# Kernel tuning notes

Hardware: AMD Instinct MI355X
Metric: run time of the kernel (lower is better)

## Reference

```python
import jax, jax.numpy as jnp
import numpy as np

N = 500_000   # mesh vertices
M = 500_000   # non-manifold sample points
K = 4         # quad-mesh valence
WEIGHTS = [7000.0, 600.0, 10.0, 50.0, 30.0, 3.0]


def setup_inputs() -> dict:
    key = jax.random.key(0)
    ks = jax.random.split(key, 11)
    return {
        "manifold_pred": jax.random.normal(ks[0], (1, N), jnp.float32),
        "nonmanifold_pred": jax.random.normal(ks[1], (1, M), jnp.float32),
        "mnfld_grad": jax.random.normal(ks[2], (1, N, 3), jnp.float32),
        "nonmnfld_grad": jax.random.normal(ks[3], (1, M, 3), jnp.float32),
        "mnfld_hessian": jax.random.normal(ks[4], (1, N, 3, 3), jnp.float32),
        "mnfld_n_gt": jax.random.normal(ks[5], (1, N, 3), jnp.float32),
        "theta": jax.random.normal(ks[6], (1, N, 1), jnp.float32),
        "local_coord_u": jax.random.normal(ks[7], (1, N, 3), jnp.float32),
        "local_coord_v": jax.random.normal(ks[8], (1, N, 3), jnp.float32),
        "rot": jax.random.normal(ks[9], (N, K, 3, 3), jnp.float32),
        "neighbors": jax.random.randint(ks[10], (N, K), 0, N, jnp.int32),
    }


def reference(manifold_pred, nonmanifold_pred, mnfld_grad, nonmnfld_grad,
              mnfld_hessian, mnfld_n_gt, theta, local_coord_u, local_coord_v,
              rot, neighbors):
    H = mnfld_hessian[0]          # [N,3,3] per-vertex hessian
    n_gt = mnfld_n_gt[0]          # [N,3]

    # morse term: n^T H  (div_type == 'l1')
    morse = 0.5 * jnp.abs(jnp.einsum('nd,nde->ne', n_gt, H)).mean()

    sdf_term = jnp.abs(manifold_pred).mean()

    # eikonal over concatenated grads (morse path uses nonmnfld_grad when near_points is None)
    all_grads = jnp.concatenate([nonmnfld_grad, mnfld_grad], axis=-2)  # [1, M+N, 3]
    eikonal_term = jnp.abs(jnp.linalg.norm(all_grads, axis=2) - 1.0).mean()

    inter_term = jnp.exp(-100.0 * jnp.abs(nonmanifold_pred)).mean()

    # cross-field directions from theta
    u, v, th = local_coord_u[0], local_coord_v[0], theta[0]  # [N,3],[N,3],[N,1]
    va = u * jnp.cos(th) + v * jnp.sin(th)
    va = va / (jnp.linalg.norm(va, axis=-1, keepdims=True) + 1e-12)
    vb = -u * jnp.sin(th) + v * jnp.cos(th)
    vb = vb / (jnp.linalg.norm(vb, axis=-1, keepdims=True) + 1e-12)

    # per-vertex (v^T H) x v hessian alignment (single valence group covers all vertices)
    vaH = jnp.einsum('nd,nde->ne', va, H)
    vbH = jnp.einsum('nd,nde->ne', vb, H)
    h_alpha = jnp.abs(jnp.cross(vaH, va)).mean()
    h_beta = jnp.abs(jnp.cross(vbH, vb)).mean()
    theta_hessian_term = 0.5 * (h_alpha + h_beta)

    # neighbor consistency: rotate neighbor cross-field into vertex frame, dot products
    vaj = jnp.einsum('nkij,nkj->nki', rot, va[neighbors])  # [N,K,3]
    vbj = jnp.einsum('nkij,nkj->nki', rot, vb[neighbors])
    aa = jnp.abs(jnp.einsum('nd,nkd->nk', va, vaj))
    ab = jnp.abs(jnp.einsum('nd,nkd->nk', va, vbj))
    ba = jnp.abs(jnp.einsum('nd,nkd->nk', vb, vaj))
    bb = jnp.abs(jnp.einsum('nd,nkd->nk', vb, vbj))
    theta_neighbors_term = (aa + ab + ba + bb - 2.0).mean()

    w = WEIGHTS
    loss = (w[0] * sdf_term + w[1] * inter_term + w[3] * eikonal_term
            + w[5] * morse + w[2] * theta_hessian_term + w[4] * theta_neighbors_term)
    return jnp.stack([loss, sdf_term, inter_term, eikonal_term, morse,
                      theta_hessian_term, theta_neighbors_term])
```

## Files before the change

### kernel.cpp

```cpp
#include <hip/hip_runtime.h>
#include <math.h>

static constexpr int BLOCK = 256;
static constexpr int WAVES = BLOCK / 64;
static constexpr int KVAL = 4;
static constexpr int TILE = 256;

typedef float f4 __attribute__((ext_vector_type(4)));
typedef int i4 __attribute__((ext_vector_type(4)));
typedef int i2 __attribute__((ext_vector_type(2)));
typedef unsigned int u2v __attribute__((ext_vector_type(2)));

__device__ __forceinline__ void norm3(float x, float y, float z,
                                      float& ox, float& oy, float& oz) {
  float inv = 1.0f / (sqrtf(x * x + y * y + z * z) + 1e-12f);
  ox = x * inv; oy = y * inv; oz = z * inv;
}

template <int NV>
__device__ __forceinline__ void block_reduce(float (&p)[NV]) {
#pragma unroll
  for (int off = 32; off > 0; off >>= 1)
#pragma unroll
    for (int q = 0; q < NV; ++q) p[q] += __shfl_down(p[q], off, 64);
  __shared__ float sm[WAVES][NV];
  int wave = threadIdx.x >> 6, lane = threadIdx.x & 63;
  if (lane == 0)
#pragma unroll
    for (int q = 0; q < NV; ++q) sm[wave][q] = p[q];
  __syncthreads();
  if (threadIdx.x == 0) {
#pragma unroll
    for (int q = 0; q < NV; ++q) {
      float t = 0.f;
#pragma unroll
      for (int w = 1; w < WAVES; ++w) t += sm[w][q];
      p[q] += t;
    }
  }
}

__device__ __forceinline__ void stage_f(float* __restrict__ dst,
                                        const float* __restrict__ src, int nf) {
  int t = threadIdx.x;
  int nf4 = nf >> 2;
  const f4* s4 = (const f4*)src;
  f4* d4 = (f4*)dst;
  for (int i = t; i < nf4; i += BLOCK) d4[i] = s4[i];
  int rem = nf & 3;
  if (t < rem) dst[nf4 * 4 + t] = src[nf4 * 4 + t];
}

__device__ __forceinline__ void stage_rot_pad(float* __restrict__ B,
                                              const float* __restrict__ src,
                                              int cs) {
  int nf4 = 9 * cs;
  const f4* s4 = (const f4*)src;
  for (int i = threadIdx.x; i < nf4; i += BLOCK) {
    f4 x = __builtin_nontemporal_load(s4 + i);
    int vtx = i / 9, r = i - 9 * vtx;
    float* d = B + vtx * 37 + r * 4;
    d[0] = x.x; d[1] = x.y; d[2] = x.z; d[3] = x.w;
  }
}

__device__ __forceinline__ void unpack8(u2v w, float* va, float* vb) {
  va[0] = __builtin_amdgcn_cvt_f32_fp8((int)w.x, 0);
  va[1] = __builtin_amdgcn_cvt_f32_fp8((int)w.x, 1);
  va[2] = __builtin_amdgcn_cvt_f32_fp8((int)w.x, 2);
  vb[0] = __builtin_amdgcn_cvt_f32_fp8((int)w.x, 3);
  vb[1] = __builtin_amdgcn_cvt_f32_fp8((int)w.y, 0);
  vb[2] = __builtin_amdgcn_cvt_f32_fp8((int)w.y, 1);
}

__global__ __launch_bounds__(BLOCK) void s1_kernel(
    const float* __restrict__ theta, const float* __restrict__ u,
    const float* __restrict__ v, u2v* __restrict__ vavb8, int N,
    const float* __restrict__ pred, const float* __restrict__ pgrad,
    const float* __restrict__ mp, const float* __restrict__ grad,
    const float* __restrict__ H, const float* __restrict__ ngt,
    float* __restrict__ part1, int nb1, int M) {
  __shared__ float B[2304];
  int t = threadIdx.x;
  long base = (long)blockIdx.x * TILE;
  float p[5] = {0.f, 0.f, 0.f, 0.f, 0.f};

  int cntM = 0, cntN = 0;
  if (base < M) { long c = (long)M - base; cntM = c > TILE ? TILE : (int)c; }
  if (base < N) { long c = (long)N - base; cntN = c > TILE ? TILE : (int)c; }

  float prv = 0.f, mpv = 0.f, thv = 0.f;
  if (t < cntM) prv = pred[base + t];
  if (t < cntN) { mpv = mp[base + t]; thv = theta[base + t]; }

  if (cntM > 0) stage_f(B, pgrad + 3 * base, 3 * cntM);
  __syncthreads();
  if (t < cntM) {
    float gx = B[3 * t], gy = B[3 * t + 1], gz = B[3 * t + 2];
    p[1] += fabsf(sqrtf(gx * gx + gy * gy + gz * gz) - 1.0f);
    p[4] += __expf(-100.0f * fabsf(prv));
  }
  __syncthreads();
  float ng0 = 0.f, ng1 = 0.f, ng2 = 0.f;
  if (cntN > 0) {
    stage_f(B, grad + 3 * base, 3 * cntN);
    stage_f(B + 768, ngt + 3 * base, 3 * cntN);
  }
  __syncthreads();
  if (t < cntN) {
    float gx = B[3 * t], gy = B[3 * t + 1], gz = B[3 * t + 2];
    p[1] += fabsf(sqrtf(gx * gx + gy * gy + gz * gz) - 1.0f);
    p[0] = fabsf(mpv);
    ng0 = B[768 + 3 * t]; ng1 = B[768 + 3 * t + 1]; ng2 = B[768 + 3 * t + 2];
  }
  __syncthreads();

  if (cntN > 0) {
    stage_f(B, u + 3 * base, 3 * cntN);
    stage_f(B + 768, v + 3 * base, 3 * cntN);
  }
  __syncthreads();
  float va[3] = {0.f, 0.f, 0.f}, vb[3] = {0.f, 0.f, 0.f};
  if (t < cntN) {
    float s, c;
    __sincosf(thv, &s, &c);
    float ux = B[3 * t], uy = B[3 * t + 1], uz = B[3 * t + 2];
    float vx = B[768 + 3 * t], vy = B[768 + 3 * t + 1], vz = B[768 + 3 * t + 2];
    norm3(ux * c + vx * s, uy * c + vy * s, uz * c + vz * s, va[0], va[1], va[2]);
    norm3(vx * c - ux * s, vy * c - uy * s, vz * c - uz * s, vb[0], vb[1], vb[2]);
    unsigned int w0 = (unsigned)__builtin_amdgcn_cvt_pk_fp8_f32(va[0], va[1], 0, false);
    w0 = (unsigned)__builtin_amdgcn_cvt_pk_fp8_f32(va[2], vb[0], (int)w0, true);
    unsigned int w1 = (unsigned)__builtin_amdgcn_cvt_pk_fp8_f32(vb[1], vb[2], 0, false);
    u2v o; o.x = w0; o.y = w1;
    __builtin_nontemporal_store(o, &vavb8[base + t]);
  }
  __syncthreads();

  if (cntN > 0) stage_f(B, H + 9 * base, 9 * cntN);
  __syncthreads();
  if (t < cntN) {
    float h[9];
#pragma unroll
    for (int q = 0; q < 9; ++q) h[q] = B[9 * t + q];
    p[2] = fabsf(ng0 * h[0] + ng1 * h[3] + ng2 * h[6]) +
           fabsf(ng0 * h[1] + ng1 * h[4] + ng2 * h[7]) +
           fabsf(ng0 * h[2] + ng1 * h[5] + ng2 * h[8]);
    float a0 = va[0] * h[0] + va[1] * h[3] + va[2] * h[6];
    float a1 = va[0] * h[1] + va[1] * h[4] + va[2] * h[7];
    float a2 = va[0] * h[2] + va[1] * h[5] + va[2] * h[8];
    float b0 = vb[0] * h[0] + vb[1] * h[3] + vb[2] * h[6];
    float b1 = vb[0] * h[1] + vb[1] * h[4] + vb[2] * h[7];
    float b2 = vb[0] * h[2] + vb[1] * h[5] + vb[2] * h[8];
    p[3] = fabsf(a1 * va[2] - a2 * va[1]) + fabsf(a2 * va[0] - a0 * va[2]) +
           fabsf(a0 * va[1] - a1 * va[0]) + fabsf(b1 * vb[2] - b2 * vb[1]) +
           fabsf(b2 * vb[0] - b0 * vb[2]) + fabsf(b0 * vb[1] - b1 * vb[0]);
  }

  block_reduce<5>(p);
  if (t == 0) {
#pragma unroll
    for (int q = 0; q < 5; ++q) part1[q * nb1 + blockIdx.x] = p[q];
  }
}

__global__ __launch_bounds__(BLOCK) void s3_kernel(
    const u2v* __restrict__ vavb8, const float* __restrict__ rot,
    const i2* __restrict__ nbr2, float* __restrict__ part2, int N) {
  __shared__ float B[128 * 37];
  int t = threadIdx.x;
  int vl = t >> 1;
  int h = t & 1;
  long base = (long)blockIdx.x * TILE;
  int cntN = 0;
  if (base < N) { long c = (long)N - base; cntN = c > TILE ? TILE : (int)c; }

  u2v wn[2][2]; u2v ws[2];
#pragma unroll
  for (int sp = 0; sp < 2; ++sp) {
    ws[sp] = u2v{0, 0};
    wn[sp][0] = u2v{0, 0};
    wn[sp][1] = u2v{0, 0};
    int lv = 128 * sp + vl;
    if (lv < cntN) {
      long n = base + lv;
      i2 jj = __builtin_nontemporal_load(&nbr2[2 * n + h]);
      wn[sp][0] = vavb8[jj.x];
      wn[sp][1] = vavb8[jj.y];
      ws[sp] = vavb8[n];
    }
  }

  float nsum = 0.f;
#pragma unroll
  for (int sp = 0; sp < 2; ++sp) {
    int cs = cntN - 128 * sp;
    if (cs < 0) cs = 0;
    if (cs > 128) cs = 128;
    if (cs > 0) stage_rot_pad(B, rot + 36 * (base + 128 * sp), cs);
    __syncthreads();
    if (vl < cs) {
      float va[3], vb[3];
      unpack8(ws[sp], va, vb);
      const float* R0 = B + 37 * vl;
#pragma unroll
      for (int kk = 0; kk < 2; ++kk) {
        int k = 2 * h + kk;
        float R[9];
#pragma unroll
        for (int q = 0; q < 9; ++q) R[q] = R0[9 * k + q];
        float pa0 = R[0] * va[0] + R[3] * va[1] + R[6] * va[2];
        float pa1 = R[1] * va[0] + R[4] * va[1] + R[7] * va[2];
        float pa2 = R[2] * va[0] + R[5] * va[1] + R[8] * va[2];
        float pb0 = R[0] * vb[0] + R[3] * vb[1] + R[6] * vb[2];
        float pb1 = R[1] * vb[0] + R[4] * vb[1] + R[7] * vb[2];
        float pb2 = R[2] * vb[0] + R[5] * vb[1] + R[8] * vb[2];
        float aj[3], bj[3];
        unpack8(wn[sp][kk], aj, bj);
        nsum += fabsf(pa0 * aj[0] + pa1 * aj[1] + pa2 * aj[2]) +
                fabsf(pa0 * bj[0] + pa1 * bj[1] + pa2 * bj[2]) +
                fabsf(pb0 * aj[0] + pb1 * aj[1] + pb2 * aj[2]) +
                fabsf(pb0 * bj[0] + pb1 * bj[1] + pb2 * bj[2]) - 2.0f;
      }
    }
    __syncthreads();
  }
  float p[1] = {nsum};
  block_reduce<1>(p);
  if (t == 0) part2[blockIdx.x] = p[0];
}

__global__ __launch_bounds__(BLOCK) void finalize_fast(
    const float* __restrict__ part1, int nb1, const float* __restrict__ part2,
    int nb2, float* __restrict__ out, int N, int M) {
  float s[6] = {0.f, 0.f, 0.f, 0.f, 0.f, 0.f};
  for (int b = threadIdx.x; b < nb1; b += BLOCK) {
#pragma unroll
    for (int q = 0; q < 5; ++q) s[q] += part1[q * nb1 + b];
  }
  for (int b = threadIdx.x; b < nb2; b += BLOCK) s[5] += part2[b];
  block_reduce<6>(s);
  if (threadIdx.x == 0) {
    float sdf = s[0] / (float)N;
    float eik = s[1] / (float)(N + M);
    float morse = 0.5f * s[2] / (3.0f * (float)N);
    float th = 0.5f * s[3] / (3.0f * (float)N);
    float inter = s[4] / (float)M;
    float nb = s[5] / ((float)N * (float)KVAL);
    float loss = 7000.0f * sdf + 600.0f * inter + 50.0f * eik + 3.0f * morse +
                 10.0f * th + 30.0f * nb;
    out[0] = loss; out[1] = sdf; out[2] = inter; out[3] = eik;
    out[4] = morse; out[5] = th; out[6] = nb;
  }
}

__device__ __forceinline__ void crossfield(const float* __restrict__ u,
                                           const float* __restrict__ v,
                                           const float* __restrict__ theta,
                                           int n, float va[3], float vb[3]) {
  float s, c;
  __sincosf(theta[n], &s, &c);
  float ux = u[3 * n], uy = u[3 * n + 1], uz = u[3 * n + 2];
  float vx = v[3 * n], vy = v[3 * n + 1], vz = v[3 * n + 2];
  norm3(ux * c + vx * s, uy * c + vy * s, uz * c + vz * s, va[0], va[1], va[2]);
  norm3(vx * c - ux * s, vy * c - uy * s, vz * c - uz * s, vb[0], vb[1], vb[2]);
}

__global__ __launch_bounds__(BLOCK) void vertex_kernel(
    const float* __restrict__ mp, const float* __restrict__ grad,
    const float* __restrict__ H, const float* __restrict__ ngt,
    const float* __restrict__ theta, const float* __restrict__ u,
    const float* __restrict__ v, const float* __restrict__ rot,
    const int* __restrict__ nbr, float* __restrict__ acc, int N) {
  int n = blockIdx.x * blockDim.x + threadIdx.x;
  float p[5] = {0.f, 0.f, 0.f, 0.f, 0.f};
  if (n < N) {
    float hh[9];
#pragma unroll
    for (int i = 0; i < 9; ++i) hh[i] = H[9 * (size_t)n + i];
    p[0] = fabsf(mp[n]);
    float gx = grad[3 * n], gy = grad[3 * n + 1], gz = grad[3 * n + 2];
    p[1] = fabsf(sqrtf(gx * gx + gy * gy + gz * gz) - 1.0f);
    float n0 = ngt[3 * n], n1 = ngt[3 * n + 1], n2 = ngt[3 * n + 2];
    p[2] = fabsf(n0 * hh[0] + n1 * hh[3] + n2 * hh[6]) +
           fabsf(n0 * hh[1] + n1 * hh[4] + n2 * hh[7]) +
           fabsf(n0 * hh[2] + n1 * hh[5] + n2 * hh[8]);
    float va[3], vb[3];
    crossfield(u, v, theta, n, va, vb);
    {
      float a0 = va[0] * hh[0] + va[1] * hh[3] + va[2] * hh[6];
      float a1 = va[0] * hh[1] + va[1] * hh[4] + va[2] * hh[7];
      float a2 = va[0] * hh[2] + va[1] * hh[5] + va[2] * hh[8];
      float b0 = vb[0] * hh[0] + vb[1] * hh[3] + vb[2] * hh[6];
      float b1 = vb[0] * hh[1] + vb[1] * hh[4] + vb[2] * hh[7];
      float b2 = vb[0] * hh[2] + vb[1] * hh[5] + vb[2] * hh[8];
      p[3] = fabsf(a1 * va[2] - a2 * va[1]) + fabsf(a2 * va[0] - a0 * va[2]) +
             fabsf(a0 * va[1] - a1 * va[0]) + fabsf(b1 * vb[2] - b2 * vb[1]) +
             fabsf(b2 * vb[0] - b0 * vb[2]) + fabsf(b0 * vb[1] - b1 * vb[0]);
    }
    float nsum = 0.f;
    const float* R = rot + (size_t)n * (KVAL * 9);
#pragma unroll
    for (int k = 0; k < KVAL; ++k) {
      int j = nbr[KVAL * (size_t)n + k];
      float vaj[3], vbj[3];
      crossfield(u, v, theta, j, vaj, vbj);
      float r0 = R[9 * k + 0], r1 = R[9 * k + 1], r2 = R[9 * k + 2];
      float r3 = R[9 * k + 3], r4 = R[9 * k + 4], r5 = R[9 * k + 5];
      float r6 = R[9 * k + 6], r7 = R[9 * k + 7], r8 = R[9 * k + 8];
      float wa0 = r0 * vaj[0] + r1 * vaj[1] + r2 * vaj[2];
      float wa1 = r3 * vaj[0] + r4 * vaj[1] + r5 * vaj[2];
      float wa2 = r6 * vaj[0] + r7 * vaj[1] + r8 * vaj[2];
      float wb0 = r0 * vbj[0] + r1 * vbj[1] + r2 * vbj[2];
      float wb1 = r3 * vbj[0] + r4 * vbj[1] + r5 * vbj[2];
      float wb2 = r6 * vbj[0] + r7 * vbj[1] + r8 * vbj[2];
      nsum += fabsf(va[0] * wa0 + va[1] * wa1 + va[2] * wa2) +
              fabsf(va[0] * wb0 + va[1] * wb1 + va[2] * wb2) +
              fabsf(vb[0] * wa0 + vb[1] * wa1 + vb[2] * wa2) +
              fabsf(vb[0] * wb0 + vb[1] * wb1 + vb[2] * wb2) - 2.0f;
    }
    p[4] = nsum;
  }
  block_reduce<5>(p);
  if (threadIdx.x == 0) {
    atomicAdd(&acc[0], p[0]); atomicAdd(&acc[1], p[1]); atomicAdd(&acc[2], p[2]);
    atomicAdd(&acc[3], p[3]); atomicAdd(&acc[4], p[4]);
  }
}

__global__ __launch_bounds__(BLOCK) void point_kernel(
    const float* __restrict__ pred, const float* __restrict__ grad,
    float* __restrict__ acc, int M) {
  int i = blockIdx.x * blockDim.x + threadIdx.x;
  float p[2] = {0.f, 0.f};
  if (i < M) {
    p[0] = __expf(-100.0f * fabsf(pred[i]));
    float gx = grad[3 * i], gy = grad[3 * i + 1], gz = grad[3 * i + 2];
    p[1] = fabsf(sqrtf(gx * gx + gy * gy + gz * gz) - 1.0f);
  }
  block_reduce<2>(p);
  if (threadIdx.x == 0) {
    atomicAdd(&acc[5], p[0]); atomicAdd(&acc[1], p[1]);
  }
}

__global__ void finalize_acc(const float* __restrict__ acc, float* __restrict__ out,
                             int N, int M) {
  if (threadIdx.x == 0 && blockIdx.x == 0) {
    float sdf = acc[0] / (float)N;
    float eik = acc[1] / (float)(N + M);
    float morse = 0.5f * acc[2] / (3.0f * (float)N);
    float th = 0.5f * acc[3] / (3.0f * (float)N);
    float nb = acc[4] / ((float)N * (float)KVAL);
    float inter = acc[5] / (float)M;
    float loss = 7000.0f * sdf + 600.0f * inter + 50.0f * eik + 3.0f * morse +
                 10.0f * th + 30.0f * nb;
    out[0] = loss; out[1] = sdf; out[2] = inter; out[3] = eik;
    out[4] = morse; out[5] = th; out[6] = nb;
  }
}

extern "C" void kernel_launch(void* const* d_in, const int* in_sizes, int n_in,
                              void* d_out, int out_size, void* d_ws, size_t ws_size,
                              hipStream_t stream) {
  const float* mp    = (const float*)d_in[0];
  const float* npred = (const float*)d_in[1];
  const float* grad  = (const float*)d_in[2];
  const float* ngrad = (const float*)d_in[3];
  const float* H     = (const float*)d_in[4];
  const float* ngt   = (const float*)d_in[5];
  const float* theta = (const float*)d_in[6];
  const float* u     = (const float*)d_in[7];
  const float* v     = (const float*)d_in[8];
  const float* rot   = (const float*)d_in[9];
  const int*   nbr   = (const int*)d_in[10];
  float* out = (float*)d_out;

  int N = in_sizes[0];
  int M = in_sizes[1];
  int mx = (N > M) ? N : M;
  int nb1 = (mx + TILE - 1) / TILE;
  int nb2 = (N + TILE - 1) / TILE;

  size_t off_vavb = 256;
  size_t off_p1 = off_vavb + (size_t)N * 8;
  size_t off_p2 = off_p1 + (size_t)5 * nb1 * 4;
  size_t need = off_p2 + (size_t)nb2 * 4;

  if (ws_size >= need) {
    u2v* vavb8   = (u2v*)((char*)d_ws + off_vavb);
    float* part1 = (float*)((char*)d_ws + off_p1);
    float* part2 = (float*)((char*)d_ws + off_p2);
    s1_kernel<<<nb1, BLOCK, 0, stream>>>(
        theta, u, v, vavb8, N, npred, ngrad, mp, grad, H, ngt, part1, nb1, M);
    s3_kernel<<<nb2, BLOCK, 0, stream>>>(
        vavb8, rot, (const i2*)nbr, part2, N);
    finalize_fast<<<1, BLOCK, 0, stream>>>(part1, nb1, part2, nb2, out, N, M);
  } else {
    float* acc = (float*)d_ws;
    (void)hipMemsetAsync(acc, 0, 6 * sizeof(float), stream);
    vertex_kernel<<<(N + BLOCK - 1) / BLOCK, BLOCK, 0, stream>>>(
        mp, grad, H, ngt, theta, u, v, rot, nbr, acc, N);
    point_kernel<<<(M + BLOCK - 1) / BLOCK, BLOCK, 0, stream>>>(npred, ngrad, acc, M);
    finalize_acc<<<1, 64, 0, stream>>>(acc, out, N, M);
  }
}
```

Before: 51.24 us.

## Split crossfield into small prepass and fuse stream terms with neighbor term

Moves crossfield computation (theta, u, v to fp8 va/vb) into a small first kernel. The streaming loss terms (sdf, eikonal, inter, morse, hessian) and the neighbor-consistency term now run together in one main kernel. That kernel issues the neighbor gathers early, so their latency overlaps with the streaming of H and the gradients. It also uses one thread per vertex with an int4 neighbor load, replacing two threads per vertex. The per-vertex va/vb for the hessian term now come from the fp8-packed values, which lowers that term's precision. The main kernel uses more shared memory (about 19KB), which may reduce occupancy.

```diff
diff --git a/kernel.cpp b/kernel.cpp
--- a/kernel.cpp
+++ b/kernel.cpp
@@ -8,7 +8,6 @@
 
 typedef float f4 __attribute__((ext_vector_type(4)));
 typedef int i4 __attribute__((ext_vector_type(4)));
-typedef int i2 __attribute__((ext_vector_type(2)));
 typedef unsigned int u2v __attribute__((ext_vector_type(2)));
 
 __device__ __forceinline__ void norm3(float x, float y, float z,
@@ -73,59 +72,27 @@
   vb[2] = __builtin_amdgcn_cvt_f32_fp8((int)w.y, 1);
 }
 
-__global__ __launch_bounds__(BLOCK) void s1_kernel(
+__global__ __launch_bounds__(BLOCK) void cf_kernel(
     const float* __restrict__ theta, const float* __restrict__ u,
-    const float* __restrict__ v, u2v* __restrict__ vavb8, int N,
-    const float* __restrict__ pred, const float* __restrict__ pgrad,
-    const float* __restrict__ mp, const float* __restrict__ grad,
-    const float* __restrict__ H, const float* __restrict__ ngt,
-    float* __restrict__ part1, int nb1, int M) {
-  __shared__ float B[2304];
+    const float* __restrict__ v, u2v* __restrict__ vavb8, int N) {
+  __shared__ float B[1536];
   int t = threadIdx.x;
   long base = (long)blockIdx.x * TILE;
-  float p[5] = {0.f, 0.f, 0.f, 0.f, 0.f};
-
-  int cntM = 0, cntN = 0;
-  if (base < M) { long c = (long)M - base; cntM = c > TILE ? TILE : (int)c; }
-  if (base < N) { long c = (long)N - base; cntN = c > TILE ? TILE : (int)c; }
-
-  float prv = 0.f, mpv = 0.f, thv = 0.f;
-  if (t < cntM) prv = pred[base + t];
-  if (t < cntN) { mpv = mp[base + t]; thv = theta[base + t]; }
-
-  if (cntM > 0) stage_f(B, pgrad + 3 * base, 3 * cntM);
-  __syncthreads();
-  if (t < cntM) {
-    float gx = B[3 * t], gy = B[3 * t + 1], gz = B[3 * t + 2];
-    p[1] += fabsf(sqrtf(gx * gx + gy * gy + gz * gz) - 1.0f);
-    p[4] += __expf(-100.0f * fabsf(prv));
-  }
-  __syncthreads();
-  float ng0 = 0.f, ng1 = 0.f, ng2 = 0.f;
-  if (cntN > 0) {
-    stage_f(B, grad + 3 * base, 3 * cntN);
-    stage_f(B + 768, ngt + 3 * base, 3 * cntN);
-  }
-  __syncthreads();
-  if (t < cntN) {
-    float gx = B[3 * t], gy = B[3 * t + 1], gz = B[3 * t + 2];
-    p[1] += fabsf(sqrtf(gx * gx + gy * gy + gz * gz) - 1.0f);
-    p[0] = fabsf(mpv);
-    ng0 = B[768 + 3 * t]; ng1 = B[768 + 3 * t + 1]; ng2 = B[768 + 3 * t + 2];
-  }
-  __syncthreads();
-
-  if (cntN > 0) {
-    stage_f(B, u + 3 * base, 3 * cntN);
-    stage_f(B + 768, v + 3 * base, 3 * cntN);
-  }
-  __syncthreads();
-  float va[3] = {0.f, 0.f, 0.f}, vb[3] = {0.f, 0.f, 0.f};
-  if (t < cntN) {
+  int cnt = 0;
+  if (base < N) { long c = (long)N - base; cnt = c > TILE ? TILE : (int)c; }
+  float thv = 0.f;
+  if (t < cnt) thv = theta[base + t];
+  if (cnt > 0) {
+    stage_f(B, u + 3 * base, 3 * cnt);
+    stage_f(B + 768, v + 3 * base, 3 * cnt);
+  }
+  __syncthreads();
+  if (t < cnt) {
     float s, c;
     __sincosf(thv, &s, &c);
     float ux = B[3 * t], uy = B[3 * t + 1], uz = B[3 * t + 2];
     float vx = B[768 + 3 * t], vy = B[768 + 3 * t + 1], vz = B[768 + 3 * t + 2];
+    float va[3], vb[3];
     norm3(ux * c + vx * s, uy * c + vy * s, uz * c + vz * s, va[0], va[1], va[2]);
     norm3(vx * c - ux * s, vy * c - uy * s, vz * c - uz * s, vb[0], vb[1], vb[2]);
     unsigned int w0 = (unsigned)__builtin_amdgcn_cvt_pk_fp8_f32(va[0], va[1], 0, false);
@@ -133,6 +100,63 @@
     unsigned int w1 = (unsigned)__builtin_amdgcn_cvt_pk_fp8_f32(vb[1], vb[2], 0, false);
     u2v o; o.x = w0; o.y = w1;
     __builtin_nontemporal_store(o, &vavb8[base + t]);
+  }
+}
+
+__global__ __launch_bounds__(BLOCK) void main_kernel(
+    const u2v* __restrict__ vavb8, int N,
+    const float* __restrict__ pred, const float* __restrict__ pgrad,
+    const float* __restrict__ mp, const float* __restrict__ grad,
+    const float* __restrict__ H, const float* __restrict__ ngt,
+    const float* __restrict__ rot, const i4* __restrict__ nbr4,
+    float* __restrict__ part, int nbb, int M) {
+  __shared__ float B[4736];
+  int t = threadIdx.x;
+  long base = (long)blockIdx.x * TILE;
+  float p[6] = {0.f, 0.f, 0.f, 0.f, 0.f, 0.f};
+
+  int cntM = 0, cntN = 0;
+  if (base < M) { long c = (long)M - base; cntM = c > TILE ? TILE : (int)c; }
+  if (base < N) { long c = (long)N - base; cntN = c > TILE ? TILE : (int)c; }
+
+  float prv = 0.f, mpv = 0.f;
+  u2v ws = u2v{0, 0};
+  u2v wn[4];
+#pragma unroll
+  for (int k = 0; k < KVAL; ++k) wn[k] = u2v{0, 0};
+  if (t < cntM) prv = pred[base + t];
+  if (t < cntN) {
+    mpv = mp[base + t];
+    ws = vavb8[base + t];
+    i4 jj = __builtin_nontemporal_load(&nbr4[base + t]);
+    wn[0] = vavb8[jj.x];
+    wn[1] = vavb8[jj.y];
+    wn[2] = vavb8[jj.z];
+    wn[3] = vavb8[jj.w];
+  }
+  float va[3], vb[3];
+  unpack8(ws, va, vb);
+
+  if (cntM > 0) stage_f(B, pgrad + 3 * base, 3 * cntM);
+  __syncthreads();
+  if (t < cntM) {
+    float gx = B[3 * t], gy = B[3 * t + 1], gz = B[3 * t + 2];
+    p[1] += fabsf(sqrtf(gx * gx + gy * gy + gz * gz) - 1.0f);
+    p[4] += __expf(-100.0f * fabsf(prv));
+  }
+  __syncthreads();
+
+  float ng0 = 0.f, ng1 = 0.f, ng2 = 0.f;
+  if (cntN > 0) {
+    stage_f(B, grad + 3 * base, 3 * cntN);
+    stage_f(B + 768, ngt + 3 * base, 3 * cntN);
+  }
+  __syncthreads();
+  if (t < cntN) {
+    float gx = B[3 * t], gy = B[3 * t + 1], gz = B[3 * t + 2];
+    p[1] += fabsf(sqrtf(gx * gx + gy * gy + gz * gz) - 1.0f);
+    p[0] = fabsf(mpv);
+    ng0 = B[768 + 3 * t]; ng1 = B[768 + 3 * t + 1]; ng2 = B[768 + 3 * t + 2];
   }
   __syncthreads();
 
@@ -155,40 +179,7 @@
            fabsf(a0 * va[1] - a1 * va[0]) + fabsf(b1 * vb[2] - b2 * vb[1]) +
            fabsf(b2 * vb[0] - b0 * vb[2]) + fabsf(b0 * vb[1] - b1 * vb[0]);
   }
-
-  block_reduce<5>(p);
-  if (t == 0) {
-#pragma unroll
-    for (int q = 0; q < 5; ++q) part1[q * nb1 + blockIdx.x] = p[q];
-  }
-}
-
-__global__ __launch_bounds__(BLOCK) void s3_kernel(
-    const u2v* __restrict__ vavb8, const float* __restrict__ rot,
-    const i2* __restrict__ nbr2, float* __restrict__ part2, int N) {
-  __shared__ float B[128 * 37];
-  int t = threadIdx.x;
-  int vl = t >> 1;
-  int h = t & 1;
-  long base = (long)blockIdx.x * TILE;
-  int cntN = 0;
-  if (base < N) { long c = (long)N - base; cntN = c > TILE ? TILE : (int)c; }
-
-  u2v wn[2][2]; u2v ws[2];
-#pragma unroll
-  for (int sp = 0; sp < 2; ++sp) {
-    ws[sp] = u2v{0, 0};
-    wn[sp][0] = u2v{0, 0};
-    wn[sp][1] = u2v{0, 0};
-    int lv = 128 * sp + vl;
-    if (lv < cntN) {
-      long n = base + lv;
-      i2 jj = __builtin_nontemporal_load(&nbr2[2 * n + h]);
-      wn[sp][0] = vavb8[jj.x];
-      wn[sp][1] = vavb8[jj.y];
-      ws[sp] = vavb8[n];
-    }
-  }
+  __syncthreads();
 
   float nsum = 0.f;
 #pragma unroll
@@ -198,13 +189,11 @@
     if (cs > 128) cs = 128;
     if (cs > 0) stage_rot_pad(B, rot + 36 * (base + 128 * sp), cs);
     __syncthreads();
-    if (vl < cs) {
-      float va[3], vb[3];
-      unpack8(ws[sp], va, vb);
-      const float* R0 = B + 37 * vl;
-#pragma unroll
-      for (int kk = 0; kk < 2; ++kk) {
-        int k = 2 * h + kk;
+    int lt = t - 128 * sp;
+    if (lt >= 0 && lt < cs) {
+      const float* R0 = B + 37 * lt;
+#pragma unroll
+      for (int k = 0; k < KVAL; ++k) {
         float R[9];
 #pragma unroll
         for (int q = 0; q < 9; ++q) R[q] = R0[9 * k + q];
@@ -215,7 +204,7 @@
         float pb1 = R[1] * vb[0] + R[4] * vb[1] + R[7] * vb[2];
         float pb2 = R[2] * vb[0] + R[5] * vb[1] + R[8] * vb[2];
         float aj[3], bj[3];
-        unpack8(wn[sp][kk], aj, bj);
+        unpack8(wn[k], aj, bj);
         nsum += fabsf(pa0 * aj[0] + pa1 * aj[1] + pa2 * aj[2]) +
                 fabsf(pa0 * bj[0] + pa1 * bj[1] + pa2 * bj[2]) +
                 fabsf(pb0 * aj[0] + pb1 * aj[1] + pb2 * aj[2]) +
@@ -224,20 +213,23 @@
     }
     __syncthreads();
   }
-  float p[1] = {nsum};
-  block_reduce<1>(p);
-  if (t == 0) part2[blockIdx.x] = p[0];
+  p[5] = nsum;
+
+  block_reduce<6>(p);
+  if (t == 0) {
+#pragma unroll
+    for (int q = 0; q < 6; ++q) part[q * nbb + blockIdx.x] = p[q];
+  }
 }
 
 __global__ __launch_bounds__(BLOCK) void finalize_fast(
-    const float* __restrict__ part1, int nb1, const float* __restrict__ part2,
-    int nb2, float* __restrict__ out, int N, int M) {
+    const float* __restrict__ part, int nbb, float* __restrict__ out,
+    int N, int M) {
   float s[6] = {0.f, 0.f, 0.f, 0.f, 0.f, 0.f};
-  for (int b = threadIdx.x; b < nb1; b += BLOCK) {
-#pragma unroll
-    for (int q = 0; q < 5; ++q) s[q] += part1[q * nb1 + b];
-  }
-  for (int b = threadIdx.x; b < nb2; b += BLOCK) s[5] += part2[b];
+  for (int b = threadIdx.x; b < nbb; b += BLOCK) {
+#pragma unroll
+    for (int q = 0; q < 6; ++q) s[q] += part[q * nbb + b];
+  }
   block_reduce<6>(s);
   if (threadIdx.x == 0) {
     float sdf = s[0] / (float)N;
@@ -378,23 +370,21 @@
   int N = in_sizes[0];
   int M = in_sizes[1];
   int mx = (N > M) ? N : M;
-  int nb1 = (mx + TILE - 1) / TILE;
-  int nb2 = (N + TILE - 1) / TILE;
+  int nbN = (N + TILE - 1) / TILE;
+  int nbb = (mx + TILE - 1) / TILE;
 
   size_t off_vavb = 256;
-  size_t off_p1 = off_vavb + (size_t)N * 8;
-  size_t off_p2 = off_p1 + (size_t)5 * nb1 * 4;
-  size_t need = off_p2 + (size_t)nb2 * 4;
+  size_t off_p = off_vavb + (size_t)N * 8;
+  size_t need = off_p + (size_t)6 * nbb * 4;
 
   if (ws_size >= need) {
-    u2v* vavb8   = (u2v*)((char*)d_ws + off_vavb);
-    float* part1 = (float*)((char*)d_ws + off_p1);
-    float* part2 = (float*)((char*)d_ws + off_p2);
-    s1_kernel<<<nb1, BLOCK, 0, stream>>>(
-        theta, u, v, vavb8, N, npred, ngrad, mp, grad, H, ngt, part1, nb1, M);
-    s3_kernel<<<nb2, BLOCK, 0, stream>>>(
-        vavb8, rot, (const i2*)nbr, part2, N);
-    finalize_fast<<<1, BLOCK, 0, stream>>>(part1, nb1, part2, nb2, out, N, M);
+    u2v* vavb8  = (u2v*)((char*)d_ws + off_vavb);
+    float* part = (float*)((char*)d_ws + off_p);
+    cf_kernel<<<nbN, BLOCK, 0, stream>>>(theta, u, v, vavb8, N);
+    main_kernel<<<nbb, BLOCK, 0, stream>>>(
+        vavb8, N, npred, ngrad, mp, grad, H, ngt, rot, (const i4*)nbr,
+        part, nbb, M);
+    finalize_fast<<<1, BLOCK, 0, stream>>>(part, nbb, out, N, M);
   } else {
     float* acc = (float*)d_ws;
     (void)hipMemsetAsync(acc, 0, 6 * sizeof(float), stream);
```

After: 53.79 us. 5.0% more time.

## Split crossfield into small kernel and merge reductions with neighbor pass

Applied to the files above, without the earlier changes.

Moves the crossfield computation (theta, u, v to packed fp8 va/vb) into a small first kernel. The per-point reductions and the neighbor-consistency pass now run together in one interleaved kernel: even blocks do the reductions and odd blocks do the neighbor term. The goal is to cut the serial dependency so the heavy streaming reductions overlap with the rot/gather neighbor work instead of waiting behind them. In exchange the reduction path reloads va/vb from the fp8 buffer, which adds extra reads and extra fp8 quantization in the hessian term. It also raises shared memory per block to the larger of the two paths.

```diff
diff --git a/kernel.cpp b/kernel.cpp
--- a/kernel.cpp
+++ b/kernel.cpp
@@ -73,59 +73,27 @@
   vb[2] = __builtin_amdgcn_cvt_f32_fp8((int)w.y, 1);
 }
 
-__global__ __launch_bounds__(BLOCK) void s1_kernel(
+__global__ __launch_bounds__(BLOCK) void cf_kernel(
     const float* __restrict__ theta, const float* __restrict__ u,
-    const float* __restrict__ v, u2v* __restrict__ vavb8, int N,
-    const float* __restrict__ pred, const float* __restrict__ pgrad,
-    const float* __restrict__ mp, const float* __restrict__ grad,
-    const float* __restrict__ H, const float* __restrict__ ngt,
-    float* __restrict__ part1, int nb1, int M) {
-  __shared__ float B[2304];
+    const float* __restrict__ v, u2v* __restrict__ vavb8, int N) {
+  __shared__ float B[1536];
   int t = threadIdx.x;
   long base = (long)blockIdx.x * TILE;
-  float p[5] = {0.f, 0.f, 0.f, 0.f, 0.f};
-
-  int cntM = 0, cntN = 0;
-  if (base < M) { long c = (long)M - base; cntM = c > TILE ? TILE : (int)c; }
-  if (base < N) { long c = (long)N - base; cntN = c > TILE ? TILE : (int)c; }
-
-  float prv = 0.f, mpv = 0.f, thv = 0.f;
-  if (t < cntM) prv = pred[base + t];
-  if (t < cntN) { mpv = mp[base + t]; thv = theta[base + t]; }
-
-  if (cntM > 0) stage_f(B, pgrad + 3 * base, 3 * cntM);
+  int cnt = 0;
+  if (base < N) { long c = (long)N - base; cnt = c > TILE ? TILE : (int)c; }
+  float thv = 0.f;
+  if (t < cnt) thv = theta[base + t];
+  if (cnt > 0) {
+    stage_f(B, u + 3 * base, 3 * cnt);
+    stage_f(B + 768, v + 3 * base, 3 * cnt);
+  }
   __syncthreads();
-  if (t < cntM) {
-    float gx = B[3 * t], gy = B[3 * t + 1], gz = B[3 * t + 2];
-    p[1] += fabsf(sqrtf(gx * gx + gy * gy + gz * gz) - 1.0f);
-    p[4] += __expf(-100.0f * fabsf(prv));
-  }
-  __syncthreads();
-  float ng0 = 0.f, ng1 = 0.f, ng2 = 0.f;
-  if (cntN > 0) {
-    stage_f(B, grad + 3 * base, 3 * cntN);
-    stage_f(B + 768, ngt + 3 * base, 3 * cntN);
-  }
-  __syncthreads();
-  if (t < cntN) {
-    float gx = B[3 * t], gy = B[3 * t + 1], gz = B[3 * t + 2];
-    p[1] += fabsf(sqrtf(gx * gx + gy * gy + gz * gz) - 1.0f);
-    p[0] = fabsf(mpv);
-    ng0 = B[768 + 3 * t]; ng1 = B[768 + 3 * t + 1]; ng2 = B[768 + 3 * t + 2];
-  }
-  __syncthreads();
-
-  if (cntN > 0) {
-    stage_f(B, u + 3 * base, 3 * cntN);
-    stage_f(B + 768, v + 3 * base, 3 * cntN);
-  }
-  __syncthreads();
-  float va[3] = {0.f, 0.f, 0.f}, vb[3] = {0.f, 0.f, 0.f};
-  if (t < cntN) {
+  if (t < cnt) {
     float s, c;
     __sincosf(thv, &s, &c);
     float ux = B[3 * t], uy = B[3 * t + 1], uz = B[3 * t + 2];
     float vx = B[768 + 3 * t], vy = B[768 + 3 * t + 1], vz = B[768 + 3 * t + 2];
+    float va[3], vb[3];
     norm3(ux * c + vx * s, uy * c + vy * s, uz * c + vz * s, va[0], va[1], va[2]);
     norm3(vx * c - ux * s, vy * c - uy * s, vz * c - uz * s, vb[0], vb[1], vb[2]);
     unsigned int w0 = (unsigned)__builtin_amdgcn_cvt_pk_fp8_f32(va[0], va[1], 0, false);
@@ -134,110 +102,149 @@
     u2v o; o.x = w0; o.y = w1;
     __builtin_nontemporal_store(o, &vavb8[base + t]);
   }
-  __syncthreads();
-
-  if (cntN > 0) stage_f(B, H + 9 * base, 9 * cntN);
-  __syncthreads();
-  if (t < cntN) {
-    float h[9];
-#pragma unroll
-    for (int q = 0; q < 9; ++q) h[q] = B[9 * t + q];
-    p[2] = fabsf(ng0 * h[0] + ng1 * h[3] + ng2 * h[6]) +
-           fabsf(ng0 * h[1] + ng1 * h[4] + ng2 * h[7]) +
-           fabsf(ng0 * h[2] + ng1 * h[5] + ng2 * h[8]);
-    float a0 = va[0] * h[0] + va[1] * h[3] + va[2] * h[6];
-    float a1 = va[0] * h[1] + va[1] * h[4] + va[2] * h[7];
-    float a2 = va[0] * h[2] + va[1] * h[5] + va[2] * h[8];
-    float b0 = vb[0] * h[0] + vb[1] * h[3] + vb[2] * h[6];
-    float b1 = vb[0] * h[1] + vb[1] * h[4] + vb[2] * h[7];
-    float b2 = vb[0] * h[2] + vb[1] * h[5] + vb[2] * h[8];
-    p[3] = fabsf(a1 * va[2] - a2 * va[1]) + fabsf(a2 * va[0] - a0 * va[2]) +
-           fabsf(a0 * va[1] - a1 * va[0]) + fabsf(b1 * vb[2] - b2 * vb[1]) +
-           fabsf(b2 * vb[0] - b0 * vb[2]) + fabsf(b0 * vb[1] - b1 * vb[0]);
-  }
-
-  block_reduce<5>(p);
-  if (t == 0) {
-#pragma unroll
-    for (int q = 0; q < 5; ++q) part1[q * nb1 + blockIdx.x] = p[q];
-  }
-}
-
-__global__ __launch_bounds__(BLOCK) void s3_kernel(
-    const u2v* __restrict__ vavb8, const float* __restrict__ rot,
-    const i2* __restrict__ nbr2, float* __restrict__ part2, int N) {
-  __shared__ float B[128 * 37];
+}
+
+__global__ __launch_bounds__(BLOCK) void mega_kernel(
+    const u2v* __restrict__ vavb8, int N,
+    const float* __restrict__ pred, const float* __restrict__ pgrad,
+    const float* __restrict__ mp, const float* __restrict__ grad,
+    const float* __restrict__ H, const float* __restrict__ ngt,
+    const float* __restrict__ rot, const i2* __restrict__ nbr2,
+    float* __restrict__ part1, float* __restrict__ part2, int nT, int M) {
+  __shared__ float B[4736];
   int t = threadIdx.x;
-  int vl = t >> 1;
-  int h = t & 1;
-  long base = (long)blockIdx.x * TILE;
-  int cntN = 0;
-  if (base < N) { long c = (long)N - base; cntN = c > TILE ? TILE : (int)c; }
-
-  u2v wn[2][2]; u2v ws[2];
-#pragma unroll
-  for (int sp = 0; sp < 2; ++sp) {
-    ws[sp] = u2v{0, 0};
-    wn[sp][0] = u2v{0, 0};
-    wn[sp][1] = u2v{0, 0};
-    int lv = 128 * sp + vl;
-    if (lv < cntN) {
-      long n = base + lv;
-      i2 jj = __builtin_nontemporal_load(&nbr2[2 * n + h]);
-      wn[sp][0] = vavb8[jj.x];
-      wn[sp][1] = vavb8[jj.y];
-      ws[sp] = vavb8[n];
-    }
-  }
-
-  float nsum = 0.f;
-#pragma unroll
-  for (int sp = 0; sp < 2; ++sp) {
-    int cs = cntN - 128 * sp;
-    if (cs < 0) cs = 0;
-    if (cs > 128) cs = 128;
-    if (cs > 0) stage_rot_pad(B, rot + 36 * (base + 128 * sp), cs);
+  int tile = blockIdx.x >> 1;
+  long base = (long)tile * TILE;
+
+  if ((blockIdx.x & 1) == 0) {
+    float p[5] = {0.f, 0.f, 0.f, 0.f, 0.f};
+    int cntM = 0, cntN = 0;
+    if (base < M) { long c = (long)M - base; cntM = c > TILE ? TILE : (int)c; }
+    if (base < N) { long c = (long)N - base; cntN = c > TILE ? TILE : (int)c; }
+
+    float prv = 0.f, mpv = 0.f;
+    u2v ws = u2v{0, 0};
+    if (t < cntM) prv = pred[base + t];
+    if (t < cntN) { mpv = mp[base + t]; ws = vavb8[base + t]; }
+    float va[3], vb[3];
+    unpack8(ws, va, vb);
+
+    if (cntM > 0) stage_f(B, pgrad + 3 * base, 3 * cntM);
     __syncthreads();
-    if (vl < cs) {
-      float va[3], vb[3];
-      unpack8(ws[sp], va, vb);
-      const float* R0 = B + 37 * vl;
-#pragma unroll
-      for (int kk = 0; kk < 2; ++kk) {
-        int k = 2 * h + kk;
-        float R[9];
-#pragma unroll
-        for (int q = 0; q < 9; ++q) R[q] = R0[9 * k + q];
-        float pa0 = R[0] * va[0] + R[3] * va[1] + R[6] * va[2];
-        float pa1 = R[1] * va[0] + R[4] * va[1] + R[7] * va[2];
-        float pa2 = R[2] * va[0] + R[5] * va[1] + R[8] * va[2];
-        float pb0 = R[0] * vb[0] + R[3] * vb[1] + R[6] * vb[2];
-        float pb1 = R[1] * vb[0] + R[4] * vb[1] + R[7] * vb[2];
-        float pb2 = R[2] * vb[0] + R[5] * vb[1] + R[8] * vb[2];
-        float aj[3], bj[3];
-        unpack8(wn[sp][kk], aj, bj);
-        nsum += fabsf(pa0 * aj[0] + pa1 * aj[1] + pa2 * aj[2]) +
-                fabsf(pa0 * bj[0] + pa1 * bj[1] + pa2 * bj[2]) +
-                fabsf(pb0 * aj[0] + pb1 * aj[1] + pb2 * aj[2]) +
-                fabsf(pb0 * bj[0] + pb1 * bj[1] + pb2 * bj[2]) - 2.0f;
+    if (t < cntM) {
+      float gx = B[3 * t], gy = B[3 * t + 1], gz = B[3 * t + 2];
+      p[1] += fabsf(sqrtf(gx * gx + gy * gy + gz * gz) - 1.0f);
+      p[4] += __expf(-100.0f * fabsf(prv));
+    }
+    __syncthreads();
+    float ng0 = 0.f, ng1 = 0.f, ng2 = 0.f;
+    if (cntN > 0) {
+      stage_f(B, grad + 3 * base, 3 * cntN);
+      stage_f(B + 768, ngt + 3 * base, 3 * cntN);
+    }
+    __syncthreads();
+    if (t < cntN) {
+      float gx = B[3 * t], gy = B[3 * t + 1], gz = B[3 * t + 2];
+      p[1] += fabsf(sqrtf(gx * gx + gy * gy + gz * gz) - 1.0f);
+      p[0] = fabsf(mpv);
+      ng0 = B[768 + 3 * t]; ng1 = B[768 + 3 * t + 1]; ng2 = B[768 + 3 * t + 2];
+    }
+    __syncthreads();
+    if (cntN > 0) stage_f(B, H + 9 * base, 9 * cntN);
+    __syncthreads();
+    if (t < cntN) {
+      float h[9];
+#pragma unroll
+      for (int q = 0; q < 9; ++q) h[q] = B[9 * t + q];
+      p[2] = fabsf(ng0 * h[0] + ng1 * h[3] + ng2 * h[6]) +
+             fabsf(ng0 * h[1] + ng1 * h[4] + ng2 * h[7]) +
+             fabsf(ng0 * h[2] + ng1 * h[5] + ng2 * h[8]);
+      float a0 = va[0] * h[0] + va[1] * h[3] + va[2] * h[6];
+      float a1 = va[0] * h[1] + va[1] * h[4] + va[2] * h[7];
+      float a2 = va[0] * h[2] + va[1] * h[5] + va[2] * h[8];
+      float b0 = vb[0] * h[0] + vb[1] * h[3] + vb[2] * h[6];
+      float b1 = vb[0] * h[1] + vb[1] * h[4] + vb[2] * h[7];
+      float b2 = vb[0] * h[2] + vb[1] * h[5] + vb[2] * h[8];
+      p[3] = fabsf(a1 * va[2] - a2 * va[1]) + fabsf(a2 * va[0] - a0 * va[2]) +
+             fabsf(a0 * va[1] - a1 * va[0]) + fabsf(b1 * vb[2] - b2 * vb[1]) +
+             fabsf(b2 * vb[0] - b0 * vb[2]) + fabsf(b0 * vb[1] - b1 * vb[0]);
+    }
+    block_reduce<5>(p);
+    if (t == 0) {
+#pragma unroll
+      for (int q = 0; q < 5; ++q) part1[q * nT + tile] = p[q];
+    }
+  } else {
+    int vl = t >> 1;
+    int h = t & 1;
+    int cntN = 0;
+    if (base < N) { long c = (long)N - base; cntN = c > TILE ? TILE : (int)c; }
+
+    u2v wn[2][2]; u2v ws[2];
+#pragma unroll
+    for (int sp = 0; sp < 2; ++sp) {
+      ws[sp] = u2v{0, 0};
+      wn[sp][0] = u2v{0, 0};
+      wn[sp][1] = u2v{0, 0};
+      int lv = 128 * sp + vl;
+      if (lv < cntN) {
+        long n = base + lv;
+        i2 jj = __builtin_nontemporal_load(&nbr2[2 * n + h]);
+        wn[sp][0] = vavb8[jj.x];
+        wn[sp][1] = vavb8[jj.y];
+        ws[sp] = vavb8[n];
       }
     }
-    __syncthreads();
-  }
-  float p[1] = {nsum};
-  block_reduce<1>(p);
-  if (t == 0) part2[blockIdx.x] = p[0];
+
+    float nsum = 0.f;
+#pragma unroll
+    for (int sp = 0; sp < 2; ++sp) {
+      int cs = cntN - 128 * sp;
+      if (cs < 0) cs = 0;
+      if (cs > 128) cs = 128;
+      if (cs > 0) stage_rot_pad(B, rot + 36 * (base + 128 * sp), cs);
+      __syncthreads();
+      if (vl < cs) {
+        float va[3], vb[3];
+        unpack8(ws[sp], va, vb);
+        const float* R0 = B + 37 * vl;
+#pragma unroll
+        for (int kk = 0; kk < 2; ++kk) {
+          int k = 2 * h + kk;
+          float R[9];
+#pragma unroll
+          for (int q = 0; q < 9; ++q) R[q] = R0[9 * k + q];
+          float pa0 = R[0] * va[0] + R[3] * va[1] + R[6] * va[2];
+          float pa1 = R[1] * va[0] + R[4] * va[1] + R[7] * va[2];
+          float pa2 = R[2] * va[0] + R[5] * va[1] + R[8] * va[2];
+          float pb0 = R[0] * vb[0] + R[3] * vb[1] + R[6] * vb[2];
+          float pb1 = R[1] * vb[0] + R[4] * vb[1] + R[7] * vb[2];
+          float pb2 = R[2] * vb[0] + R[5] * vb[1] + R[8] * vb[2];
+          float aj[3], bj[3];
+          unpack8(wn[sp][kk], aj, bj);
+          nsum += fabsf(pa0 * aj[0] + pa1 * aj[1] + pa2 * aj[2]) +
+                  fabsf(pa0 * bj[0] + pa1 * bj[1] + pa2 * bj[2]) +
+                  fabsf(pb0 * aj[0] + pb1 * aj[1] + pb2 * aj[2]) +
+                  fabsf(pb0 * bj[0] + pb1 * bj[1] + pb2 * bj[2]) - 2.0f;
+        }
+      }
+      __syncthreads();
+    }
+    float p[1] = {nsum};
+    block_reduce<1>(p);
+    if (t == 0) part2[tile] = p[0];
+  }
 }
 
 __global__ __launch_bounds__(BLOCK) void finalize_fast(
-    const float* __restrict__ part1, int nb1, const float* __restrict__ part2,
-    int nb2, float* __restrict__ out, int N, int M) {
+    const float* __restrict__ part1, const float* __restrict__ part2, int nT,
+    float* __restrict__ out, int N, int M) {
   float s[6] = {0.f, 0.f, 0.f, 0.f, 0.f, 0.f};
-  for (int b = threadIdx.x; b < nb1; b += BLOCK) {
-#pragma unroll
-    for (int q = 0; q < 5; ++q) s[q] += part1[q * nb1 + b];
-  }
-  for (int b = threadIdx.x; b < nb2; b += BLOCK) s[5] += part2[b];
+  for (int b = threadIdx.x; b < nT; b += BLOCK) {
+#pragma unroll
+    for (int q = 0; q < 5; ++q) s[q] += part1[q * nT + b];
+    s[5] += part2[b];
+  }
   block_reduce<6>(s);
   if (threadIdx.x == 0) {
     float sdf = s[0] / (float)N;
@@ -378,23 +385,23 @@
   int N = in_sizes[0];
   int M = in_sizes[1];
   int mx = (N > M) ? N : M;
-  int nb1 = (mx + TILE - 1) / TILE;
-  int nb2 = (N + TILE - 1) / TILE;
+  int nT = (mx + TILE - 1) / TILE;
+  int nbN = (N + TILE - 1) / TILE;
 
   size_t off_vavb = 256;
   size_t off_p1 = off_vavb + (size_t)N * 8;
-  size_t off_p2 = off_p1 + (size_t)5 * nb1 * 4;
-  size_t need = off_p2 + (size_t)nb2 * 4;
+  size_t off_p2 = off_p1 + (size_t)5 * nT * 4;
+  size_t need = off_p2 + (size_t)nT * 4;
 
   if (ws_size >= need) {
     u2v* vavb8   = (u2v*)((char*)d_ws + off_vavb);
     float* part1 = (float*)((char*)d_ws + off_p1);
     float* part2 = (float*)((char*)d_ws + off_p2);
-    s1_kernel<<<nb1, BLOCK, 0, stream>>>(
-        theta, u, v, vavb8, N, npred, ngrad, mp, grad, H, ngt, part1, nb1, M);
-    s3_kernel<<<nb2, BLOCK, 0, stream>>>(
-        vavb8, rot, (const i2*)nbr, part2, N);
-    finalize_fast<<<1, BLOCK, 0, stream>>>(part1, nb1, part2, nb2, out, N, M);
+    cf_kernel<<<nbN, BLOCK, 0, stream>>>(theta, u, v, vavb8, N);
+    mega_kernel<<<2 * nT, BLOCK, 0, stream>>>(
+        vavb8, N, npred, ngrad, mp, grad, H, ngt, rot, (const i2*)nbr,
+        part1, part2, nT, M);
+    finalize_fast<<<1, BLOCK, 0, stream>>>(part1, part2, nT, out, N, M);
   } else {
     float* acc = (float*)d_ws;
     (void)hipMemsetAsync(acc, 0, 6 * sizeof(float), stream);
```

Measured after the change: 60.93 us. 1.19x slower.
